# Optimization experiments

Hardware: AMD Instinct MI355X
Metric: run time of the kernel (lower is better)

The kernel has to match this reference:

```python
import jax, jax.numpy as jnp
import numpy as np

EPS = 1e-8  # RMSNormMultiHead default eps (forward passes self.eps)


def rms_norm_multihead(x, weight):
    # x: (B, L, H, d); normalize over last dim in float32, then scale per (H, d)
    x32 = x.astype(jnp.float32)
    normed = x32 * jax.lax.rsqrt(jnp.mean(x32 * x32, axis=-1, keepdims=True) + EPS)
    return normed.astype(x.dtype) * weight


def setup_inputs() -> dict:
    key = jax.random.key(0)
    k0, k1, k2 = jax.random.split(key, 3)
    B, L, D, H = 2, 1024, 1024, 16
    d = D // H
    X = jax.random.normal(k0, (B, L, D), dtype=jnp.float32)
    Wq = jax.random.normal(k1, (D, D), dtype=jnp.float32) * 0.02  # q_proj weight (out, in)
    Wv = jax.random.normal(k2, (D, D), dtype=jnp.float32) * 0.02  # v_proj weight (out, in)
    q_norm_w = jnp.ones((H, d), dtype=jnp.float32)
    v_norm_w = jnp.ones((H, d), dtype=jnp.float32)
    return {"X": X, "Wq": Wq, "Wv": Wv, "q_norm_w": q_norm_w, "v_norm_w": v_norm_w}


def reference(X, Wq, Wv, q_norm_w, v_norm_w):
    B, L, D = X.shape
    H, d = q_norm_w.shape
    K = X.reshape(B, L, H, d)
    Q = rms_norm_multihead((X @ Wq.T).reshape(B, L, H, d), q_norm_w)
    V = rms_norm_multihead((X @ Wv.T).reshape(B, L, H, d), v_norm_w)
    # cumulative outer-product KV state: (B, L, H, d, e)
    W = jnp.cumsum(jnp.einsum('blhd,blhe->blhde', K, V), axis=1)
    out = jnp.einsum('blhd,blhde->blhe', Q, W).reshape(B, L, D)
    return out
```

## Files before the change

kernel.cpp:

```cpp
#include <hip/hip_runtime.h>

#define BB 2
#define LL 1024
#define DD 1024
#define HH 16
#define NC 16
#define EPSF 1e-8f

typedef __attribute__((ext_vector_type(8))) short bf16x8;
typedef __attribute__((ext_vector_type(4))) float f32x4;
typedef unsigned short u16;

static __device__ inline u16 f2bf(float f) {
    unsigned int u = __builtin_bit_cast(unsigned int, f);
    u += 0x7fff + ((u >> 16) & 1);
    return (u16)(u >> 16);
}
static __device__ inline float bf2f(u16 v) {
    unsigned int u = ((unsigned int)v) << 16;
    return __builtin_bit_cast(float, u);
}
static __device__ inline void gload_lds16(const u16* g, u16* l) {
    __builtin_amdgcn_global_load_lds((const __attribute__((address_space(1))) void*)g,
                                     (__attribute__((address_space(3))) void*)l, 16, 0, 0);
}

__global__ __launch_bounds__(256) void cvt_k(const float* __restrict__ X,
                                             const float* __restrict__ Wq,
                                             const float* __restrict__ Wv,
                                             u16* __restrict__ Xb,
                                             u16* __restrict__ Wqb,
                                             u16* __restrict__ Wvb)
{
    int i = (blockIdx.x * 256 + threadIdx.x) * 4;
    const float* s; u16* d; int off;
    if (i < 2*1024*1024)      { s = X;  d = Xb;  off = i; }
    else if (i < 3*1024*1024) { s = Wq; d = Wqb; off = i - 2*1024*1024; }
    else                      { s = Wv; d = Wvb; off = i - 3*1024*1024; }
    float4 v = *(const float4*)(s + off);
    ushort4 o;
    o.x = f2bf(v.x); o.y = f2bf(v.y); o.z = f2bf(v.z); o.w = f2bf(v.w);
    *(ushort4*)(d + off) = o;
}

__global__ __launch_bounds__(256) void gemm_fused(const u16* __restrict__ Xb,
                                                  const u16* __restrict__ Wqb,
                                                  const u16* __restrict__ Wvb,
                                                  const float* __restrict__ qw,
                                                  const float* __restrict__ vw,
                                                  u16* __restrict__ Qb,
                                                  u16* __restrict__ Vb,
                                                  u16* __restrict__ S)
{
    const int K = DD, N = DD;
    const int nb = (blockIdx.x & 7) * 64 + (blockIdx.x >> 3);
    const int z = nb >> 8;
    const int m0 = ((nb >> 4) & 15) * 128, n0 = (nb & 15) * 64;
    const u16* W = z ? Wvb : Wqb;
    const float* nw = z ? vw : qw;
    u16* Y = z ? Vb : Qb;

    __shared__ alignas(16) char smem[49152];
    u16* Ab = (u16*)smem;
    u16* Bb = (u16*)(smem + 32768);

    const int tid = threadIdx.x, w = tid >> 6, lane = tid & 63;
    const int quad = lane >> 4, l16 = lane & 15;

    const int lr8 = lane >> 3;
    const int lc8 = (lane & 7) ^ lr8;
    const u16* gA = Xb + (size_t)(m0 + w*32 + lr8) * K + lc8 * 8;
    const u16* gB = W  + (size_t)(n0 + w*16 + lr8) * K + lc8 * 8;

    f32x4 acc[2][4] = {};

    auto stage = [&](int buf, int k0) {
        u16* As = Ab + buf * (128*64);
        u16* Bs = Bb + buf * (64*64);
        #pragma unroll
        for (int q = 0; q < 4; ++q)
            gload_lds16(gA + k0 + (size_t)q*8*K, As + (w*32 + q*8)*64);
        #pragma unroll
        for (int q = 0; q < 2; ++q)
            gload_lds16(gB + k0 + (size_t)q*8*K, Bs + (w*16 + q*8)*64);
    };
    auto compute = [&](int buf) {
        const u16* As = Ab + buf * (128*64);
        const u16* Bs = Bb + buf * (64*64);
        #pragma unroll
        for (int hh = 0; hh < 2; ++hh) {
            const int co = (((hh << 2) | quad) ^ (l16 & 7)) * 8;
            bf16x8 af[2], bfr[4];
            #pragma unroll
            for (int i = 0; i < 2; ++i)
                af[i] = *(const bf16x8*)&As[(w*32 + i*16 + l16) * 64 + co];
            #pragma unroll
            for (int j = 0; j < 4; ++j)
                bfr[j] = *(const bf16x8*)&Bs[(j*16 + l16) * 64 + co];
            #pragma unroll
            for (int i = 0; i < 2; ++i)
                #pragma unroll
                for (int j = 0; j < 4; ++j)
                    acc[i][j] = __builtin_amdgcn_mfma_f32_16x16x32_bf16(af[i], bfr[j], acc[i][j], 0, 0, 0);
        }
    };

    stage(0, 0);
    __syncthreads();
    int cur = 0;
    for (int k0 = 0; k0 < K; k0 += 64) {
        if (k0 + 64 < K) stage(cur ^ 1, k0 + 64);
        compute(cur);
        __syncthreads();
        cur ^= 1;
    }

    u16 (*Vt)[136] = (u16 (*)[136])smem;
    u16 (*Kt)[136] = (u16 (*)[136])(smem + 17408);

    float wv4[4];
    #pragma unroll
    for (int j = 0; j < 4; ++j) wv4[j] = nw[n0 + j*16 + l16];
    #pragma unroll
    for (int i = 0; i < 2; ++i) {
        float ss[4];
        #pragma unroll
        for (int r = 0; r < 4; ++r) {
            float s = 0.f;
            #pragma unroll
            for (int j = 0; j < 4; ++j) s += acc[i][j][r] * acc[i][j][r];
            ss[r] = s;
        }
        #pragma unroll
        for (int off = 1; off < 16; off <<= 1)
            #pragma unroll
            for (int r = 0; r < 4; ++r) ss[r] += __shfl_xor(ss[r], off, 64);
        float sc[4];
        #pragma unroll
        for (int r = 0; r < 4; ++r) sc[r] = rsqrtf(ss[r] * (1.f/64.f) + EPSF);
        #pragma unroll
        for (int r = 0; r < 4; ++r) {
            u16* yp = Y + (size_t)(m0 + w*32 + i*16 + quad*4 + r) * N + n0;
            #pragma unroll
            for (int j = 0; j < 4; ++j) {
                u16 val = f2bf(acc[i][j][r] * sc[r] * wv4[j]);
                yp[j*16 + l16] = val;
                if (z)
                    Vt[j*16 + l16][w*32 + i*16 + quad*4 + r] = val;
            }
        }
    }

    if (z) {
        {
            const int row = tid >> 1, q2 = tid & 1;
            size_t gb = (size_t)(m0 + row) * DD + n0 + q2 * 32;
            u16 kk[32];
            #pragma unroll
            for (int i2 = 0; i2 < 32; i2 += 4)
                *(ushort4*)&kk[i2] = *(const ushort4*)(Xb + gb + i2);
            #pragma unroll
            for (int i2 = 0; i2 < 32; ++i2)
                Kt[q2*32 + i2][row] = kk[i2];
        }
        __syncthreads();
        const int me = (w & 1) * 32, nd = (w >> 1) * 32;
        const int bb_ = m0 >> 10, c0 = (m0 & 1023) >> 6, h = nb & 15;
        const int bh = bb_ * HH + h;
        #pragma unroll
        for (int cc = 0; cc < 2; ++cc) {
            f32x4 sacc[2][2] = {};
            #pragma unroll
            for (int k0 = 0; k0 < 64; k0 += 32) {
                bf16x8 av[2], bv[2];
                #pragma unroll
                for (int i2 = 0; i2 < 2; ++i2)
                    av[i2] = *(const bf16x8*)&Vt[me + i2*16 + l16][cc*64 + k0 + quad*8];
                #pragma unroll
                for (int j2 = 0; j2 < 2; ++j2)
                    bv[j2] = *(const bf16x8*)&Kt[nd + j2*16 + l16][cc*64 + k0 + quad*8];
                #pragma unroll
                for (int i2 = 0; i2 < 2; ++i2)
                    #pragma unroll
                    for (int j2 = 0; j2 < 2; ++j2)
                        sacc[i2][j2] = __builtin_amdgcn_mfma_f32_16x16x32_bf16(av[i2], bv[j2], sacc[i2][j2], 0, 0, 0);
            }
            u16* Sp = S + ((size_t)((bh << 4) | (c0 + cc)) << 12) + w*1024;
            #pragma unroll
            for (int i2 = 0; i2 < 2; ++i2)
                #pragma unroll
                for (int j2 = 0; j2 < 2; ++j2)
                    #pragma unroll
                    for (int r = 0; r < 4; ++r)
                        Sp[(i2*2 + j2)*256 + r*64 + lane] = f2bf(sacc[i2][j2][r]);
        }
    }
}

__global__ __launch_bounds__(256) void out_k2(const u16* __restrict__ Xb,
                                              const u16* __restrict__ Qb,
                                              const u16* __restrict__ Vb,
                                              const u16* __restrict__ S,
                                              float* __restrict__ out)
{
    const int nb = (blockIdx.x & 7) * 64 + (blockIdx.x >> 3);
    const int c = 15 - (nb & 15);
    const int bh = nb >> 4;
    const int h = bh & 15, b = bh >> 4;
    __shared__ u16 Qs[64][72];
    __shared__ u16 Ks[64][72];
    __shared__ u16 Vt[64][72];
    __shared__ u16 St[64][72];
    const int tid = threadIdx.x;
    {
        const int row = tid >> 2, q = tid & 3;
        size_t gbase = (size_t)(b*LL + c*64 + row) * DD + h*64 + q*16;
        u16 vv[16];
        #pragma unroll
        for (int i = 0; i < 16; i += 4) {
            *(ushort4*)&Qs[row][q*16 + i] = *(const ushort4*)(Qb + gbase + i);
            *(ushort4*)&Ks[row][q*16 + i] = *(const ushort4*)(Xb + gbase + i);
            *(ushort4*)&vv[i] = *(const ushort4*)(Vb + gbase + i);
        }
        #pragma unroll
        for (int i = 0; i < 16; ++i)
            Vt[q*16 + i][row] = vv[i];
        float facc[16] = {};
        const u16* Sbase = S + ((size_t)(bh * NC) << 12);
        int cp = 0;
        for (; cp + 4 <= c; cp += 4) {
            ushort4 sv[4][4];
            #pragma unroll
            for (int u = 0; u < 4; ++u)
                #pragma unroll
                for (int jj = 0; jj < 4; ++jj)
                    sv[u][jj] = *(const ushort4*)(Sbase + ((size_t)(cp + u) << 12) + tid*4 + jj*1024);
            #pragma unroll
            for (int u = 0; u < 4; ++u)
                #pragma unroll
                for (int jj = 0; jj < 4; ++jj) {
                    facc[jj*4+0] += bf2f(sv[u][jj].x);
                    facc[jj*4+1] += bf2f(sv[u][jj].y);
                    facc[jj*4+2] += bf2f(sv[u][jj].z);
                    facc[jj*4+3] += bf2f(sv[u][jj].w);
                }
        }
        for (; cp < c; ++cp) {
            const u16* Sc = Sbase + ((size_t)cp << 12);
            #pragma unroll
            for (int jj = 0; jj < 4; ++jj) {
                ushort4 sv = *(const ushort4*)(Sc + tid*4 + jj*1024);
                facc[jj*4+0] += bf2f(sv.x);
                facc[jj*4+1] += bf2f(sv.y);
                facc[jj*4+2] += bf2f(sv.z);
                facc[jj*4+3] += bf2f(sv.w);
            }
        }
        #pragma unroll
        for (int jj = 0; jj < 4; ++jj) {
            int g = tid * 4;
            int ij = (g >> 8) & 3, r = (g >> 6) & 3, ln = g & 63;
            int e = (jj & 1)*32 + (ij >> 1)*16 + (ln >> 4)*4 + r;
            int d = (jj >> 1)*32 + (ij & 1)*16 + (ln & 15);
            ushort4 o;
            o.x = f2bf(facc[jj*4+0]);
            o.y = f2bf(facc[jj*4+1]);
            o.z = f2bf(facc[jj*4+2]);
            o.w = f2bf(facc[jj*4+3]);
            *(ushort4*)&St[e][d] = o;
        }
    }
    __syncthreads();
    const int w = tid >> 6, lane = tid & 63, quad = lane >> 4, l16 = lane & 15;
    const int mo = (w & 1) * 32, no = (w >> 1) * 32;

    f32x4 pacc[2][2] = {};
    #pragma unroll
    for (int k0 = 0; k0 < 64; k0 += 32) {
        bf16x8 aq[2], bk[2];
        #pragma unroll
        for (int i = 0; i < 2; ++i)
            aq[i] = *(const bf16x8*)&Qs[mo + i*16 + l16][k0 + quad*8];
        #pragma unroll
        for (int j = 0; j < 2; ++j)
            bk[j] = *(const bf16x8*)&Ks[no + j*16 + l16][k0 + quad*8];
        #pragma unroll
        for (int i = 0; i < 2; ++i)
            #pragma unroll
            for (int j = 0; j < 2; ++j)
                pacc[i][j] = __builtin_amdgcn_mfma_f32_16x16x32_bf16(aq[i], bk[j], pacc[i][j], 0, 0, 0);
    }
    __syncthreads();
    #pragma unroll
    for (int i = 0; i < 2; ++i)
        #pragma unroll
        for (int j = 0; j < 2; ++j)
            #pragma unroll
            for (int r = 0; r < 4; ++r) {
                int l  = mo + i*16 + quad*4 + r;
                int lp = no + j*16 + l16;
                Ks[l][lp] = (lp <= l) ? f2bf(pacc[i][j][r]) : (u16)0;
            }
    __syncthreads();

    f32x4 acc[2][2] = {};
    #pragma unroll
    for (int k0 = 0; k0 < 64; k0 += 32) {
        bf16x8 a1[2], b1[2], a2[2], b2[2];
        #pragma unroll
        for (int i = 0; i < 2; ++i) {
            a1[i] = *(const bf16x8*)&Ks[mo + i*16 + l16][k0 + quad*8];
            a2[i] = *(const bf16x8*)&Qs[mo + i*16 + l16][k0 + quad*8];
        }
        #pragma unroll
        for (int j = 0; j < 2; ++j) {
            b1[j] = *(const bf16x8*)&Vt[no + j*16 + l16][k0 + quad*8];
            b2[j] = *(const bf16x8*)&St[no + j*16 + l16][k0 + quad*8];
        }
        #pragma unroll
        for (int i = 0; i < 2; ++i)
            #pragma unroll
            for (int j = 0; j < 2; ++j) {
                acc[i][j] = __builtin_amdgcn_mfma_f32_16x16x32_bf16(a1[i], b1[j], acc[i][j], 0, 0, 0);
                acc[i][j] = __builtin_amdgcn_mfma_f32_16x16x32_bf16(a2[i], b2[j], acc[i][j], 0, 0, 0);
            }
    }
    float* op = out + (size_t)(b*LL + c*64) * DD + h*64;
    #pragma unroll
    for (int i = 0; i < 2; ++i)
        #pragma unroll
        for (int j = 0; j < 2; ++j)
            #pragma unroll
            for (int r = 0; r < 4; ++r)
                op[(size_t)(mo + i*16 + quad*4 + r) * DD + no + j*16 + l16] = acc[i][j][r];
}

extern "C" void kernel_launch(void* const* d_in, const int* in_sizes, int n_in,
                              void* d_out, int out_size, void* d_ws, size_t ws_size,
                              hipStream_t stream) {
    const float* X  = (const float*)d_in[0];
    const float* Wq = (const float*)d_in[1];
    const float* Wv = (const float*)d_in[2];
    const float* qw = (const float*)d_in[3];
    const float* vw = (const float*)d_in[4];
    float* out = (float*)d_out;

    u16* Xb  = (u16*)d_ws;
    u16* Wqb = Xb  + (size_t)2*1024*1024;
    u16* Wvb = Wqb + (size_t)1024*1024;
    u16* Qb  = Wvb + (size_t)1024*1024;
    u16* Vb  = Qb  + (size_t)2*1024*1024;
    u16* S   = Vb  + (size_t)2*1024*1024;

    cvt_k<<<4096, 256, 0, stream>>>(X, Wq, Wv, Xb, Wqb, Wvb);
    gemm_fused<<<512, 256, 0, stream>>>(Xb, Wqb, Wvb, qw, vw, Qb, Vb, S);
    out_k2<<<512, 256, 0, stream>>>(Xb, Qb, Vb, S, out);
}
```

Before: 98.05 us.

## Enlarge GEMM tile to 128x128 and restructure fused chunk-state epilogue

The fused projection GEMM now uses 128x128 output tiles with a 2x2 warp layout (each warp computes 64x64), halving the grid to 256 blocks and raising data reuse per loaded tile. The epilogue chunk-state computation is rewritten to handle two heads per block, with each warp producing a full 64x64 state for one head/chunk pair. It also drops the XCD-interleaved block index remapping in both kernels. The trade-off is more LDS (68KB) and accumulator registers per block, plus fewer blocks, which lowers occupancy and may leave CUs idle on a 256-CU device.

Result: slower. 102.8 us (+4.8%).

```diff
diff --git a/kernel.cpp b/kernel.cpp
--- a/kernel.cpp
+++ b/kernel.cpp
@@ -53,52 +53,53 @@
                                                   u16* __restrict__ S)
 {
     const int K = DD, N = DD;
-    const int nb = (blockIdx.x & 7) * 64 + (blockIdx.x >> 3);
-    const int z = nb >> 8;
-    const int m0 = ((nb >> 4) & 15) * 128, n0 = (nb & 15) * 64;
+    const int nb = blockIdx.x;
+    const int z  = nb >> 7;
+    const int mt = (nb >> 3) & 15, nt = nb & 7;
+    const int m0 = mt * 128, n0 = nt * 128;
     const u16* W = z ? Wvb : Wqb;
     const float* nw = z ? vw : qw;
     u16* Y = z ? Vb : Qb;
 
-    __shared__ alignas(16) char smem[49152];
+    __shared__ alignas(16) char smem[69632];
     u16* Ab = (u16*)smem;
     u16* Bb = (u16*)(smem + 32768);
 
     const int tid = threadIdx.x, w = tid >> 6, lane = tid & 63;
     const int quad = lane >> 4, l16 = lane & 15;
+    const int wr = w >> 1, wc = w & 1;
 
     const int lr8 = lane >> 3;
     const int lc8 = (lane & 7) ^ lr8;
     const u16* gA = Xb + (size_t)(m0 + w*32 + lr8) * K + lc8 * 8;
-    const u16* gB = W  + (size_t)(n0 + w*16 + lr8) * K + lc8 * 8;
-
-    f32x4 acc[2][4] = {};
+    const u16* gB = W  + (size_t)(n0 + w*32 + lr8) * K + lc8 * 8;
+
+    f32x4 acc[4][4] = {};
 
     auto stage = [&](int buf, int k0) {
         u16* As = Ab + buf * (128*64);
-        u16* Bs = Bb + buf * (64*64);
-        #pragma unroll
-        for (int q = 0; q < 4; ++q)
+        u16* Bs = Bb + buf * (128*64);
+        #pragma unroll
+        for (int q = 0; q < 4; ++q) {
             gload_lds16(gA + k0 + (size_t)q*8*K, As + (w*32 + q*8)*64);
-        #pragma unroll
-        for (int q = 0; q < 2; ++q)
-            gload_lds16(gB + k0 + (size_t)q*8*K, Bs + (w*16 + q*8)*64);
+            gload_lds16(gB + k0 + (size_t)q*8*K, Bs + (w*32 + q*8)*64);
+        }
     };
     auto compute = [&](int buf) {
         const u16* As = Ab + buf * (128*64);
-        const u16* Bs = Bb + buf * (64*64);
+        const u16* Bs = Bb + buf * (128*64);
         #pragma unroll
         for (int hh = 0; hh < 2; ++hh) {
             const int co = (((hh << 2) | quad) ^ (l16 & 7)) * 8;
-            bf16x8 af[2], bfr[4];
-            #pragma unroll
-            for (int i = 0; i < 2; ++i)
-                af[i] = *(const bf16x8*)&As[(w*32 + i*16 + l16) * 64 + co];
+            bf16x8 af[4], bfr[4];
+            #pragma unroll
+            for (int i = 0; i < 4; ++i)
+                af[i] = *(const bf16x8*)&As[(wr*64 + i*16 + l16) * 64 + co];
             #pragma unroll
             for (int j = 0; j < 4; ++j)
-                bfr[j] = *(const bf16x8*)&Bs[(j*16 + l16) * 64 + co];
-            #pragma unroll
-            for (int i = 0; i < 2; ++i)
+                bfr[j] = *(const bf16x8*)&Bs[(wc*64 + j*16 + l16) * 64 + co];
+            #pragma unroll
+            for (int i = 0; i < 4; ++i)
                 #pragma unroll
                 for (int j = 0; j < 4; ++j)
                     acc[i][j] = __builtin_amdgcn_mfma_f32_16x16x32_bf16(af[i], bfr[j], acc[i][j], 0, 0, 0);
@@ -115,14 +116,15 @@
         cur ^= 1;
     }
 
-    u16 (*Vt)[136] = (u16 (*)[136])smem;
-    u16 (*Kt)[136] = (u16 (*)[136])(smem + 17408);
-
+    u16 (*Vt)[64][136] = (u16 (*)[64][136])smem;
+    u16 (*Kt)[64][136] = (u16 (*)[64][136])(smem + 34816);
+
+    const int hcol = n0 + wc*64;
     float wv4[4];
     #pragma unroll
-    for (int j = 0; j < 4; ++j) wv4[j] = nw[n0 + j*16 + l16];
-    #pragma unroll
-    for (int i = 0; i < 2; ++i) {
+    for (int j = 0; j < 4; ++j) wv4[j] = nw[hcol + j*16 + l16];
+    #pragma unroll
+    for (int i = 0; i < 4; ++i) {
         float ss[4];
         #pragma unroll
         for (int r = 0; r < 4; ++r) {
@@ -140,60 +142,60 @@
         for (int r = 0; r < 4; ++r) sc[r] = rsqrtf(ss[r] * (1.f/64.f) + EPSF);
         #pragma unroll
         for (int r = 0; r < 4; ++r) {
-            u16* yp = Y + (size_t)(m0 + w*32 + i*16 + quad*4 + r) * N + n0;
+            const int lrow = wr*64 + i*16 + quad*4 + r;
+            u16* yp = Y + (size_t)(m0 + lrow) * N + hcol;
             #pragma unroll
             for (int j = 0; j < 4; ++j) {
                 u16 val = f2bf(acc[i][j][r] * sc[r] * wv4[j]);
                 yp[j*16 + l16] = val;
                 if (z)
-                    Vt[j*16 + l16][w*32 + i*16 + quad*4 + r] = val;
+                    Vt[wc][j*16 + l16][lrow] = val;
             }
         }
     }
 
     if (z) {
-        {
-            const int row = tid >> 1, q2 = tid & 1;
-            size_t gb = (size_t)(m0 + row) * DD + n0 + q2 * 32;
+        #pragma unroll
+        for (int rr = 0; rr < 2; ++rr) {
+            const int row = rr*64 + (tid >> 2), q = tid & 3;
+            size_t gb = (size_t)(m0 + row) * DD + n0 + q * 32;
             u16 kk[32];
             #pragma unroll
             for (int i2 = 0; i2 < 32; i2 += 4)
                 *(ushort4*)&kk[i2] = *(const ushort4*)(Xb + gb + i2);
             #pragma unroll
             for (int i2 = 0; i2 < 32; ++i2)
-                Kt[q2*32 + i2][row] = kk[i2];
+                Kt[q >> 1][(q & 1)*32 + i2][row] = kk[i2];
         }
         __syncthreads();
-        const int me = (w & 1) * 32, nd = (w >> 1) * 32;
-        const int bb_ = m0 >> 10, c0 = (m0 & 1023) >> 6, h = nb & 15;
-        const int bh = bb_ * HH + h;
-        #pragma unroll
-        for (int cc = 0; cc < 2; ++cc) {
-            f32x4 sacc[2][2] = {};
-            #pragma unroll
-            for (int k0 = 0; k0 < 64; k0 += 32) {
-                bf16x8 av[2], bv[2];
-                #pragma unroll
-                for (int i2 = 0; i2 < 2; ++i2)
-                    av[i2] = *(const bf16x8*)&Vt[me + i2*16 + l16][cc*64 + k0 + quad*8];
-                #pragma unroll
-                for (int j2 = 0; j2 < 2; ++j2)
-                    bv[j2] = *(const bf16x8*)&Kt[nd + j2*16 + l16][cc*64 + k0 + quad*8];
-                #pragma unroll
-                for (int i2 = 0; i2 < 2; ++i2)
-                    #pragma unroll
-                    for (int j2 = 0; j2 < 2; ++j2)
-                        sacc[i2][j2] = __builtin_amdgcn_mfma_f32_16x16x32_bf16(av[i2], bv[j2], sacc[i2][j2], 0, 0, 0);
-            }
-            u16* Sp = S + ((size_t)((bh << 4) | (c0 + cc)) << 12) + w*1024;
-            #pragma unroll
-            for (int i2 = 0; i2 < 2; ++i2)
-                #pragma unroll
-                for (int j2 = 0; j2 < 2; ++j2)
-                    #pragma unroll
-                    for (int r = 0; r < 4; ++r)
-                        Sp[(i2*2 + j2)*256 + r*64 + lane] = f2bf(sacc[i2][j2][r]);
-        }
+        const int h2 = w & 1, cc = w >> 1;
+        f32x4 sacc[4][4] = {};
+        #pragma unroll
+        for (int k0 = 0; k0 < 64; k0 += 32) {
+            bf16x8 av[4], bv[4];
+            #pragma unroll
+            for (int i2 = 0; i2 < 4; ++i2)
+                av[i2] = *(const bf16x8*)&Vt[h2][i2*16 + l16][cc*64 + k0 + quad*8];
+            #pragma unroll
+            for (int j2 = 0; j2 < 4; ++j2)
+                bv[j2] = *(const bf16x8*)&Kt[h2][j2*16 + l16][cc*64 + k0 + quad*8];
+            #pragma unroll
+            for (int i2 = 0; i2 < 4; ++i2)
+                #pragma unroll
+                for (int j2 = 0; j2 < 4; ++j2)
+                    sacc[i2][j2] = __builtin_amdgcn_mfma_f32_16x16x32_bf16(av[i2], bv[j2], sacc[i2][j2], 0, 0, 0);
+        }
+        const int bb_ = m0 >> 10, c0 = (m0 & 1023) >> 6;
+        const int bh = bb_ * HH + nt*2 + h2;
+        u16* Sp = S + ((size_t)((bh << 4) | (c0 + cc)) << 12);
+        #pragma unroll
+        for (int i2 = 0; i2 < 4; ++i2)
+            #pragma unroll
+            for (int j2 = 0; j2 < 4; ++j2)
+                #pragma unroll
+                for (int r = 0; r < 4; ++r)
+                    Sp[(((j2 >> 1)*2 + (i2 >> 1))*1024)
+                       + ((i2 & 1)*2 + (j2 & 1))*256 + r*64 + lane] = f2bf(sacc[i2][j2][r]);
     }
 }
 
@@ -203,9 +205,8 @@
                                               const u16* __restrict__ S,
                                               float* __restrict__ out)
 {
-    const int nb = (blockIdx.x & 7) * 64 + (blockIdx.x >> 3);
-    const int c = 15 - (nb & 15);
-    const int bh = nb >> 4;
+    const int c = 15 - (blockIdx.x & 15);
+    const int bh = blockIdx.x >> 4;
     const int h = bh & 15, b = bh >> 4;
     __shared__ u16 Qs[64][72];
     __shared__ u16 Ks[64][72];
@@ -353,6 +354,6 @@
     u16* S   = Vb  + (size_t)2*1024*1024;
 
     cvt_k<<<4096, 256, 0, stream>>>(X, Wq, Wv, Xb, Wqb, Wvb);
-    gemm_fused<<<512, 256, 0, stream>>>(Xb, Wqb, Wvb, qw, vw, Qb, Vb, S);
-    out_k2<<<512, 256, 0, stream>>>(Xb, Qb, Vb, S, out);
-}
+    gemm_fused<<<256, 256, 0, stream>>>(Xb, Wqb, Wvb, qw, vw, Qb, Vb, S);
+    out_k2<<<BB*HH*NC, 256, 0, stream>>>(Xb, Qb, Vb, S, out);
+}
```
